# Optimization experiments

Hardware: AMD Instinct MI355X
Metric: run time of the kernel (lower is better)

The kernel has to match this reference:

```python
import jax, jax.numpy as jnp
import numpy as np

B, N, DIM, H, DH, MLP, L = 4, 1024, 1024, 16, 64, 4096, 2
C = DIM // 4  # conditioning dim = 256


def setup_inputs() -> dict:
    key = jax.random.key(0)
    ks = jax.random.split(key, 12)
    s = 0.02
    return dict(
        x=jax.random.normal(ks[0], (B, N, DIM), jnp.float32),
        mu=jax.random.normal(ks[1], (B, N, C), jnp.float32),
        f=jax.random.normal(ks[2], (B, N, C), jnp.float32),
        Wqkv=jax.random.normal(ks[3], (L, DIM, 3 * H * DH), jnp.float32) * s,
        Wout=jax.random.normal(ks[4], (L, H * DH, DIM), jnp.float32) * s,
        bout=jnp.zeros((L, DIM), jnp.float32),
        W1=jax.random.normal(ks[5], (L, DIM, MLP), jnp.float32) * s,
        b1=jnp.zeros((L, MLP), jnp.float32),
        W2=jax.random.normal(ks[6], (L, MLP, DIM), jnp.float32) * s,
        b2=jnp.zeros((L, DIM), jnp.float32),
        Wmu=jax.random.normal(ks[7], (L, C, 6 * C), jnp.float32) * s,
        bmu=jnp.zeros((L, 6 * C), jnp.float32),
        Wf=jax.random.normal(ks[8], (L, C, 6 * 3 * C), jnp.float32) * s,
        bf=jnp.zeros((L, 6 * 3 * C), jnp.float32),
        g1=jnp.ones((L, DIM), jnp.float32),
        be1=jnp.zeros((L, DIM), jnp.float32),
        g2=jnp.ones((L, DIM), jnp.float32),
        be2=jnp.zeros((L, DIM), jnp.float32),
    )


def _ln(x, g, b):
    m = jnp.mean(x, -1, keepdims=True)
    v = jnp.mean((x - m) ** 2, -1, keepdims=True)
    return (x - m) * jax.lax.rsqrt(v + 1e-5) * g + b


def reference(x, mu, f, Wqkv, Wout, bout, W1, b1, W2, b2, Wmu, bmu, Wf, bf, g1, be1, g2, be2):
    scale = DH ** -0.5
    smu = jax.nn.silu(mu)  # SiLU applied to raw conditioning, shared across layers
    sf = jax.nn.silu(f)
    for i in range(L):
        mm = smu @ Wmu[i] + bmu[i]          # [B,N,6*C]
        mf = sf @ Wf[i] + bf[i]             # [B,N,6*3*C]
        mus = jnp.split(mm, 6, axis=-1)     # each [B,N,C]
        fs = jnp.split(mf, 6, axis=-1)      # each [B,N,3C]
        sh_a, sc_a, ga_a, sh_m, sc_m, ga_m = [
            jnp.concatenate([a, b_], -1) for a, b_ in zip(mus, fs)
        ]                                   # each [B,N,DIM]
        # attention branch
        h = _ln(x, g1[i], be1[i]) * (1 + sc_a) + sh_a
        qkv = h @ Wqkv[i]                   # [B,N,3*H*DH]
        q, k, v = [t.reshape(B, N, H, DH) for t in jnp.split(qkv, 3, axis=-1)]
        att = jax.nn.softmax(jnp.einsum('bihd,bjhd->bhij', q, k) * scale, axis=-1)
        o = jnp.einsum('bhij,bjhd->bihd', att, v).reshape(B, N, H * DH)
        x = x + ga_a * (o @ Wout[i] + bout[i])
        # MLP branch
        h2 = _ln(x, g2[i], be2[i]) * (1 + sc_m) + sh_m
        mlp = jax.nn.gelu(h2 @ W1[i] + b1[i], approximate=False) @ W2[i] + b2[i]
        x = x + ga_m * mlp
    return x
```

## Files before the change

kernel.cpp:

```cpp
#include <hip/hip_runtime.h>
#include <math.h>

#define BB 4
#define NN 1024
#define DIMD 1024
#define HHN 16
#define DHH 64
#define MLPD 4096
#define LLN 2
#define CCD 256
#define BNROWS (BB*NN)

typedef __attribute__((ext_vector_type(8))) _Float16 h8;
typedef __attribute__((ext_vector_type(4))) _Float16 h4;
typedef __attribute__((ext_vector_type(4))) float f32x4;

#define GLD16(gp, lp) __builtin_amdgcn_global_load_lds( \
    (const __attribute__((address_space(1))) void*)(gp), \
    (__attribute__((address_space(3))) void*)(lp), 16, 0, 0)

__global__ __launch_bounds__(256) void silu_kernel(const float* __restrict__ in,
                                                   _Float16* __restrict__ out, int n4) {
  int i = blockIdx.x * 256 + threadIdx.x;
  if (i < n4) {
    float4 v = ((const float4*)in)[i];
    h4 o;
    o[0] = (_Float16)(v.x / (1.f + __expf(-v.x)));
    o[1] = (_Float16)(v.y / (1.f + __expf(-v.y)));
    o[2] = (_Float16)(v.z / (1.f + __expf(-v.z)));
    o[3] = (_Float16)(v.w / (1.f + __expf(-v.w)));
    ((h4*)out)[i] = o;
  }
}

__global__ __launch_bounds__(256) void transpose_cast(const float* __restrict__ in,
                                                      _Float16* __restrict__ out,
                                                      int K, int N) {
  __shared__ float tile[32][33];
  int bx = blockIdx.x * 32;
  int by = blockIdx.y * 32;
  int tx = threadIdx.x, ty = threadIdx.y;
  #pragma unroll
  for (int r = 0; r < 32; r += 8)
    tile[ty + r][tx] = in[(size_t)(by + ty + r) * N + bx + tx];
  __syncthreads();
  #pragma unroll
  for (int r = 0; r < 32; r += 8)
    out[(size_t)(bx + ty + r) * K + by + tx] = (_Float16)tile[tx][ty + r];
}

template <int EPI, int BNT>
__global__ __launch_bounds__(256) void gemm_bt(
    const _Float16* __restrict__ A, const _Float16* __restrict__ Bt,
    int M, int Nt, int K,
    const float* __restrict__ bias,
    _Float16* __restrict__ outh,
    float* __restrict__ xio,
    const _Float16* __restrict__ mmb, const _Float16* __restrict__ mfb, int gchunk) {
  constexpr int NREP = BNT / 32;
  __shared__ _Float16 As[2][128 * 32];
  __shared__ _Float16 Bs[2][BNT * 32];
  const int tid = threadIdx.x;
  const int wave = tid >> 6, lane = tid & 63;
  const int brow = blockIdx.x * 128, bcol = blockIdx.y * BNT;
  const int wr = (wave >> 1) * 64, wc = (wave & 1) * (BNT / 2);
  const int r = lane & 15, g = lane >> 4;
  f32x4 acc[4][NREP];
  #pragma unroll
  for (int m = 0; m < 4; m++)
    #pragma unroll
    for (int n = 0; n < NREP; n++) acc[m][n] = (f32x4){0.f, 0.f, 0.f, 0.f};

  const _Float16* gA = A + (size_t)(brow + wave * 32 + (lane >> 2)) * K + (lane & 3) * 8;
  const _Float16* gB = Bt + (size_t)(bcol + wave * (BNT / 4) + (lane >> 2)) * K + (lane & 3) * 8;

  auto STAGE = [&](int b, int k0) {
    GLD16(gA + k0, &As[b][wave * 1024]);
    GLD16(gA + k0 + 16 * (size_t)K, &As[b][wave * 1024 + 512]);
    if (BNT == 128) {
      GLD16(gB + k0, &Bs[b][wave * 1024]);
      GLD16(gB + k0 + 16 * (size_t)K, &Bs[b][wave * 1024 + 512]);
    } else {
      GLD16(gB + k0, &Bs[b][wave * 512]);
    }
  };

  STAGE(0, 0);
  int cur = 0;
  for (int k0 = 0; k0 < K; k0 += 32) {
    __syncthreads();
    if (k0 + 32 < K) STAGE(cur ^ 1, k0 + 32);
    h8 af[4], bfr[NREP];
    #pragma unroll
    for (int m = 0; m < 4; m++) af[m] = *(const h8*)(&As[cur][(wr + m * 16 + r) * 32 + g * 8]);
    #pragma unroll
    for (int n = 0; n < NREP; n++) bfr[n] = *(const h8*)(&Bs[cur][(wc + n * 16 + r) * 32 + g * 8]);
    #pragma unroll
    for (int m = 0; m < 4; m++)
      #pragma unroll
      for (int n = 0; n < NREP; n++)
        acc[m][n] = __builtin_amdgcn_mfma_f32_16x16x32_f16(af[m], bfr[n], acc[m][n], 0, 0, 0);
    cur ^= 1;
  }

  #pragma unroll
  for (int n = 0; n < NREP; n++) {
    const int gcol = bcol + wc + n * 16 + r;
    const float bv = bias ? bias[gcol] : 0.f;
    #pragma unroll
    for (int m = 0; m < 4; m++) {
      const int growb = brow + wr + m * 16 + 4 * g;
      #pragma unroll
      for (int q = 0; q < 4; q++) {
        float v = acc[m][n][q] + bv;
        const size_t grow = (size_t)(growb + q);
        if (EPI == 0) {
          outh[grow * Nt + gcol] = (_Float16)v;
        } else if (EPI == 1) {
          float t = 0.5f * v * (1.f + erff(v * 0.70710678118f));
          outh[grow * Nt + gcol] = (_Float16)t;
        } else {
          float gaw = (gcol < CCD)
              ? (float)mmb[grow * (6 * CCD) + gchunk * CCD + gcol]
              : (float)mfb[grow * (18 * CCD) + gchunk * (3 * CCD) + (gcol - CCD)];
          xio[grow * DIMD + gcol] += gaw * v;
        }
      }
    }
  }
}

__global__ __launch_bounds__(256) void ln_mod(const float* __restrict__ x,
                                              const float* __restrict__ gam,
                                              const float* __restrict__ bet,
                                              const _Float16* __restrict__ mmb,
                                              const _Float16* __restrict__ mfb,
                                              int jsh, int jsc,
                                              _Float16* __restrict__ hout) {
  const int row = blockIdx.x;
  const int tid = threadIdx.x;
  const float* xr = x + (size_t)row * DIMD;
  float4 v = ((const float4*)xr)[tid];
  float s = v.x + v.y + v.z + v.w;
  float sq = v.x * v.x + v.y * v.y + v.z * v.z + v.w * v.w;
  #pragma unroll
  for (int off = 32; off > 0; off >>= 1) {
    s += __shfl_down(s, off);
    sq += __shfl_down(sq, off);
  }
  __shared__ float red[8];
  int wv = tid >> 6, ln = tid & 63;
  if (ln == 0) { red[wv] = s; red[4 + wv] = sq; }
  __syncthreads();
  s = red[0] + red[1] + red[2] + red[3];
  sq = red[4] + red[5] + red[6] + red[7];
  float mean = s * (1.f / DIMD);
  float var = sq * (1.f / DIMD) - mean * mean;
  float rs = rsqrtf(var + 1e-5f);
  int c0 = tid * 4;
  float4 gm = ((const float4*)gam)[tid];
  float4 bt = ((const float4*)bet)[tid];
  float xv[4] = {v.x, v.y, v.z, v.w};
  float gv[4] = {gm.x, gm.y, gm.z, gm.w};
  float bv[4] = {bt.x, bt.y, bt.z, bt.w};
  h4 o;
  #pragma unroll
  for (int i = 0; i < 4; i++) {
    int c = c0 + i;
    float lnv = (xv[i] - mean) * rs * gv[i] + bv[i];
    float shv, scv;
    if (c < CCD) {
      shv = (float)mmb[(size_t)row * (6 * CCD) + jsh * CCD + c];
      scv = (float)mmb[(size_t)row * (6 * CCD) + jsc * CCD + c];
    } else {
      shv = (float)mfb[(size_t)row * (18 * CCD) + jsh * (3 * CCD) + (c - CCD)];
      scv = (float)mfb[(size_t)row * (18 * CCD) + jsc * (3 * CCD) + (c - CCD)];
    }
    o[i] = (_Float16)(lnv * (1.f + scv) + shv);
  }
  *((h4*)(hout + (size_t)row * DIMD + c0)) = o;
}

__global__ __launch_bounds__(256) void attn_kernel(const _Float16* __restrict__ qkv,
                                                   _Float16* __restrict__ o) {
  __shared__ _Float16 Vs[64 * 64];
  __shared__ _Float16 Ps[4][16 * 72];
  const int bh = blockIdx.y;
  const int b = bh >> 4, hh = bh & 15;
  const int tid = threadIdx.x;
  const int wave = tid >> 6, lane = tid & 63;
  const int r = lane & 15, g = lane >> 4;
  const int RS = 3 * HHN * DHH;
  const _Float16* qb = qkv + (size_t)b * NN * RS + hh * DHH;
  const _Float16* kb = qb + HHN * DHH;
  const _Float16* vb = qb + 2 * HHN * DHH;
  const int q0 = blockIdx.x * 64 + wave * 16;

  h8 qf[2];
  qf[0] = *(const h8*)(qb + (size_t)(q0 + r) * RS + g * 8);
  qf[1] = *(const h8*)(qb + (size_t)(q0 + r) * RS + 32 + g * 8);

  f32x4 oacc[4];
  #pragma unroll
  for (int n = 0; n < 4; n++) oacc[n] = (f32x4){0.f, 0.f, 0.f, 0.f};
  float mrun[4] = {-1e30f, -1e30f, -1e30f, -1e30f};
  float lrun[4] = {0.f, 0.f, 0.f, 0.f};
  const float scale = 0.125f;

  for (int kt = 0; kt < NN / 64; ++kt) {
    const int k0 = kt * 64;
    __syncthreads();
    {
      int id = wave * 64 + lane;
      GLD16(vb + (size_t)(k0 + (id >> 3)) * RS + (id & 7) * 8, Vs + wave * 512);
      int id2 = id + 256;
      GLD16(vb + (size_t)(k0 + (id2 >> 3)) * RS + (id2 & 7) * 8, Vs + 2048 + wave * 512);
    }
    f32x4 sfr[4];
    #pragma unroll
    for (int n = 0; n < 4; n++) sfr[n] = (f32x4){0.f, 0.f, 0.f, 0.f};
    #pragma unroll
    for (int n = 0; n < 4; n++) {
      h8 kf0 = *(const h8*)(kb + (size_t)(k0 + n * 16 + r) * RS + g * 8);
      h8 kf1 = *(const h8*)(kb + (size_t)(k0 + n * 16 + r) * RS + 32 + g * 8);
      sfr[n] = __builtin_amdgcn_mfma_f32_16x16x32_f16(qf[0], kf0, sfr[n], 0, 0, 0);
      sfr[n] = __builtin_amdgcn_mfma_f32_16x16x32_f16(qf[1], kf1, sfr[n], 0, 0, 0);
    }
    float pm[4];
    #pragma unroll
    for (int q = 0; q < 4; q++)
      pm[q] = fmaxf(fmaxf(sfr[0][q], sfr[1][q]), fmaxf(sfr[2][q], sfr[3][q])) * scale;
    #pragma unroll
    for (int off = 1; off < 16; off <<= 1)
      #pragma unroll
      for (int q = 0; q < 4; q++) pm[q] = fmaxf(pm[q], __shfl_xor(pm[q], off));
    float fac[4], rsum[4];
    #pragma unroll
    for (int q = 0; q < 4; q++) {
      float mn = fmaxf(mrun[q], pm[q]);
      fac[q] = __expf(mrun[q] - mn);
      mrun[q] = mn;
      rsum[q] = 0.f;
    }
    #pragma unroll
    for (int n = 0; n < 4; n++)
      #pragma unroll
      for (int q = 0; q < 4; q++) {
        float p = __expf(sfr[n][q] * scale - mrun[q]);
        sfr[n][q] = p;
        rsum[q] += p;
      }
    #pragma unroll
    for (int off = 1; off < 16; off <<= 1)
      #pragma unroll
      for (int q = 0; q < 4; q++) rsum[q] += __shfl_xor(rsum[q], off);
    #pragma unroll
    for (int q = 0; q < 4; q++) lrun[q] = lrun[q] * fac[q] + rsum[q];
    #pragma unroll
    for (int n = 0; n < 4; n++)
      #pragma unroll
      for (int q = 0; q < 4; q++) oacc[n][q] *= fac[q];
    _Float16* Pw = Ps[wave];
    #pragma unroll
    for (int n = 0; n < 4; n++)
      #pragma unroll
      for (int q = 0; q < 4; q++)
        Pw[(4 * g + q) * 72 + n * 16 + r] = (_Float16)sfr[n][q];
    __syncthreads();
    h8 pa[2];
    pa[0] = *(const h8*)(Pw + r * 72 + g * 8);
    pa[1] = *(const h8*)(Pw + r * 72 + 32 + g * 8);
    #pragma unroll
    for (int nd = 0; nd < 4; nd++) {
      #pragma unroll
      for (int c = 0; c < 2; c++) {
        h8 vf;
        #pragma unroll
        for (int j = 0; j < 8; j++) vf[j] = Vs[(c * 32 + 8 * g + j) * 64 + nd * 16 + r];
        oacc[nd] = __builtin_amdgcn_mfma_f32_16x16x32_f16(pa[c], vf, oacc[nd], 0, 0, 0);
      }
    }
  }
  #pragma unroll
  for (int nd = 0; nd < 4; nd++)
    #pragma unroll
    for (int q = 0; q < 4; q++) {
      int row = q0 + 4 * g + q;
      int col = hh * DHH + nd * 16 + r;
      o[((size_t)b * NN + row) * DIMD + col] = (_Float16)(oacc[nd][q] / lrun[q]);
    }
}

extern "C" void kernel_launch(void* const* d_in, const int* in_sizes, int n_in,
                              void* d_out, int out_size, void* d_ws, size_t ws_size,
                              hipStream_t stream) {
  (void)in_sizes; (void)n_in; (void)out_size; (void)ws_size;
  const float* mu   = (const float*)d_in[1];
  const float* f_in = (const float*)d_in[2];
  const float* Wqkv = (const float*)d_in[3];
  const float* Wout = (const float*)d_in[4];
  const float* bout = (const float*)d_in[5];
  const float* W1   = (const float*)d_in[6];
  const float* b1   = (const float*)d_in[7];
  const float* W2   = (const float*)d_in[8];
  const float* b2   = (const float*)d_in[9];
  const float* Wmu  = (const float*)d_in[10];
  const float* bmu  = (const float*)d_in[11];
  const float* Wf   = (const float*)d_in[12];
  const float* bfv  = (const float*)d_in[13];
  const float* g1   = (const float*)d_in[14];
  const float* be1  = (const float*)d_in[15];
  const float* g2   = (const float*)d_in[16];
  const float* be2  = (const float*)d_in[17];
  float* xout = (float*)d_out;

  char* ws = (char*)d_ws;
  size_t off = 0;
  auto alloc = [&](size_t elems) -> _Float16* {
    _Float16* p = (_Float16*)(ws + off);
    off += ((elems * 2 + 255) / 256) * 256;
    return p;
  };
  _Float16* wTqkv = alloc((size_t)LLN * 3072 * 1024);
  _Float16* wTout = alloc((size_t)LLN * 1024 * 1024);
  _Float16* wT1   = alloc((size_t)LLN * 4096 * 1024);
  _Float16* wT2   = alloc((size_t)LLN * 1024 * 4096);
  _Float16* wTmu  = alloc((size_t)LLN * 1536 * 256);
  _Float16* wTf   = alloc((size_t)LLN * 4608 * 256);
  _Float16* smu   = alloc((size_t)BNROWS * CCD);
  _Float16* sfb   = alloc((size_t)BNROWS * CCD);
  _Float16* mmb   = alloc((size_t)BNROWS * 6 * CCD);
  _Float16* mfb   = alloc((size_t)BNROWS * 18 * CCD);
  _Float16* hbuf  = alloc((size_t)BNROWS * DIMD);
  _Float16* qkvb  = alloc((size_t)BNROWS * 3 * DIMD);
  _Float16* obuf  = alloc((size_t)BNROWS * DIMD);
  _Float16* m1b   = alloc((size_t)BNROWS * MLPD);

  hipMemcpyAsync(d_out, d_in[0], (size_t)BNROWS * DIMD * sizeof(float),
                 hipMemcpyDeviceToDevice, stream);

  silu_kernel<<<BNROWS * CCD / 4 / 256, 256, 0, stream>>>(mu, smu, BNROWS * CCD / 4);
  silu_kernel<<<BNROWS * CCD / 4 / 256, 256, 0, stream>>>(f_in, sfb, BNROWS * CCD / 4);

  dim3 tb(32, 8);
  for (int l = 0; l < LLN; l++) {
    transpose_cast<<<dim3(3072 / 32, 1024 / 32), tb, 0, stream>>>(
        Wqkv + (size_t)l * 1024 * 3072, wTqkv + (size_t)l * 3072 * 1024, 1024, 3072);
    transpose_cast<<<dim3(1024 / 32, 1024 / 32), tb, 0, stream>>>(
        Wout + (size_t)l * 1024 * 1024, wTout + (size_t)l * 1024 * 1024, 1024, 1024);
    transpose_cast<<<dim3(4096 / 32, 1024 / 32), tb, 0, stream>>>(
        W1 + (size_t)l * 1024 * 4096, wT1 + (size_t)l * 4096 * 1024, 1024, 4096);
    transpose_cast<<<dim3(1024 / 32, 4096 / 32), tb, 0, stream>>>(
        W2 + (size_t)l * 4096 * 1024, wT2 + (size_t)l * 1024 * 4096, 4096, 1024);
    transpose_cast<<<dim3(1536 / 32, 256 / 32), tb, 0, stream>>>(
        Wmu + (size_t)l * 256 * 1536, wTmu + (size_t)l * 1536 * 256, 256, 1536);
    transpose_cast<<<dim3(4608 / 32, 256 / 32), tb, 0, stream>>>(
        Wf + (size_t)l * 256 * 4608, wTf + (size_t)l * 4608 * 256, 256, 4608);
  }

  for (int l = 0; l < LLN; l++) {
    gemm_bt<0, 64><<<dim3(BNROWS / 128, 1536 / 64), 256, 0, stream>>>(
        smu, wTmu + (size_t)l * 1536 * 256, BNROWS, 1536, 256,
        bmu + (size_t)l * 1536, mmb, nullptr, nullptr, nullptr, 0);
    gemm_bt<0, 128><<<dim3(BNROWS / 128, 4608 / 128), 256, 0, stream>>>(
        sfb, wTf + (size_t)l * 4608 * 256, BNROWS, 4608, 256,
        bfv + (size_t)l * 4608, mfb, nullptr, nullptr, nullptr, 0);
    ln_mod<<<BNROWS, 256, 0, stream>>>(xout, g1 + (size_t)l * DIMD, be1 + (size_t)l * DIMD,
                                       mmb, mfb, 0, 1, hbuf);
    gemm_bt<0, 128><<<dim3(BNROWS / 128, 3072 / 128), 256, 0, stream>>>(
        hbuf, wTqkv + (size_t)l * 3072 * 1024, BNROWS, 3072, 1024,
        nullptr, qkvb, nullptr, nullptr, nullptr, 0);
    attn_kernel<<<dim3(NN / 64, BB * HHN), 256, 0, stream>>>(qkvb, obuf);
    gemm_bt<2, 64><<<dim3(BNROWS / 128, 1024 / 64), 256, 0, stream>>>(
        obuf, wTout + (size_t)l * 1024 * 1024, BNROWS, 1024, 1024,
        bout + (size_t)l * DIMD, nullptr, xout, mmb, mfb, 2);
    ln_mod<<<BNROWS, 256, 0, stream>>>(xout, g2 + (size_t)l * DIMD, be2 + (size_t)l * DIMD,
                                       mmb, mfb, 3, 4, hbuf);
    gemm_bt<1, 128><<<dim3(BNROWS / 128, 4096 / 128), 256, 0, stream>>>(
        hbuf, wT1 + (size_t)l * 4096 * 1024, BNROWS, 4096, 1024,
        b1 + (size_t)l * MLPD, m1b, nullptr, nullptr, nullptr, 0);
    gemm_bt<2, 64><<<dim3(BNROWS / 128, 1024 / 64), 256, 0, stream>>>(
        m1b, wT2 + (size_t)l * 1024 * 4096, BNROWS, 1024, 4096,
        b2 + (size_t)l * DIMD, nullptr, xout, mmb, mfb, 5);
  }
}
```

Measured before the change: 760.0 us.

## Pre-transpose V for attention and vectorize weight transpose-cast kernel

Adds a v_transpose kernel that writes V per head in a [d][n] layout. The attention kernel can then load V MFMA fragments straight from global memory as contiguous h8 vectors. This removes the per-tile LDS staging of V, the scalar gathers from LDS, and both block-wide __syncthreads per key tile. The weight transpose_cast kernel also moves to 64x64 tiles with float4 loads and h4 stores. The cost is an extra kernel launch and an extra write and read of V per layer, and V fragments now come from global memory or cache instead of LDS.

Result: slower. 819.2 us (+7.8%).

```diff
diff --git a/kernel.cpp b/kernel.cpp
--- a/kernel.cpp
+++ b/kernel.cpp
@@ -36,17 +36,46 @@
 __global__ __launch_bounds__(256) void transpose_cast(const float* __restrict__ in,
                                                       _Float16* __restrict__ out,
                                                       int K, int N) {
-  __shared__ float tile[32][33];
-  int bx = blockIdx.x * 32;
-  int by = blockIdx.y * 32;
-  int tx = threadIdx.x, ty = threadIdx.y;
-  #pragma unroll
-  for (int r = 0; r < 32; r += 8)
-    tile[ty + r][tx] = in[(size_t)(by + ty + r) * N + bx + tx];
+  __shared__ float tile[64][68];
+  int bx = blockIdx.x * 64;
+  int by = blockIdx.y * 64;
+  int tid = threadIdx.x;
+  int r0 = tid >> 4, c4 = (tid & 15) * 4;
+  #pragma unroll
+  for (int i = 0; i < 4; i++) {
+    float4 v = *(const float4*)(in + (size_t)(by + r0 + i * 16) * N + bx + c4);
+    *(float4*)&tile[r0 + i * 16][c4] = v;
+  }
   __syncthreads();
   #pragma unroll
-  for (int r = 0; r < 32; r += 8)
-    out[(size_t)(bx + ty + r) * K + by + tx] = (_Float16)tile[tx][ty + r];
+  for (int i = 0; i < 4; i++) {
+    int orow = r0 + i * 16;
+    h4 o;
+    #pragma unroll
+    for (int j = 0; j < 4; j++) o[j] = (_Float16)tile[c4 + j][orow];
+    *(h4*)(out + (size_t)(bx + orow) * K + by + c4) = o;
+  }
+}
+
+__global__ __launch_bounds__(256) void v_transpose(const _Float16* __restrict__ qkv,
+                                                   _Float16* __restrict__ vt) {
+  __shared__ _Float16 t[64][72];
+  int n0 = blockIdx.x * 64;
+  int bh = blockIdx.y;
+  int b = bh >> 4;
+  const _Float16* src = qkv + (size_t)b * NN * 3072 + 2048 + (bh & 15) * 64;
+  int tid = threadIdx.x;
+  int row = tid >> 2, c0 = (tid & 3) * 16;
+  *(h8*)&t[row][c0] = *(const h8*)(src + (size_t)(n0 + row) * 3072 + c0);
+  *(h8*)&t[row][c0 + 8] = *(const h8*)(src + (size_t)(n0 + row) * 3072 + c0 + 8);
+  __syncthreads();
+  int d = tid >> 2, ns = (tid & 3) * 16;
+  h8 o0, o1;
+  #pragma unroll
+  for (int j = 0; j < 8; j++) { o0[j] = t[ns + j][d]; o1[j] = t[ns + 8 + j][d]; }
+  _Float16* dst = vt + ((size_t)bh * 64 + d) * NN + n0 + ns;
+  *(h8*)dst = o0;
+  *(h8*)(dst + 8) = o1;
 }
 
 template <int EPI, int BNT>
@@ -182,8 +211,8 @@
 }
 
 __global__ __launch_bounds__(256) void attn_kernel(const _Float16* __restrict__ qkv,
+                                                   const _Float16* __restrict__ vt,
                                                    _Float16* __restrict__ o) {
-  __shared__ _Float16 Vs[64 * 64];
   __shared__ _Float16 Ps[4][16 * 72];
   const int bh = blockIdx.y;
   const int b = bh >> 4, hh = bh & 15;
@@ -193,7 +222,7 @@
   const int RS = 3 * HHN * DHH;
   const _Float16* qb = qkv + (size_t)b * NN * RS + hh * DHH;
   const _Float16* kb = qb + HHN * DHH;
-  const _Float16* vb = qb + 2 * HHN * DHH;
+  const _Float16* vtb = vt + (size_t)bh * DHH * NN;
   const int q0 = blockIdx.x * 64 + wave * 16;
 
   h8 qf[2];
@@ -206,16 +235,10 @@
   float mrun[4] = {-1e30f, -1e30f, -1e30f, -1e30f};
   float lrun[4] = {0.f, 0.f, 0.f, 0.f};
   const float scale = 0.125f;
+  _Float16* Pw = Ps[wave];
 
   for (int kt = 0; kt < NN / 64; ++kt) {
     const int k0 = kt * 64;
-    __syncthreads();
-    {
-      int id = wave * 64 + lane;
-      GLD16(vb + (size_t)(k0 + (id >> 3)) * RS + (id & 7) * 8, Vs + wave * 512);
-      int id2 = id + 256;
-      GLD16(vb + (size_t)(k0 + (id2 >> 3)) * RS + (id2 & 7) * 8, Vs + 2048 + wave * 512);
-    }
     f32x4 sfr[4];
     #pragma unroll
     for (int n = 0; n < 4; n++) sfr[n] = (f32x4){0.f, 0.f, 0.f, 0.f};
@@ -260,13 +283,11 @@
     for (int n = 0; n < 4; n++)
       #pragma unroll
       for (int q = 0; q < 4; q++) oacc[n][q] *= fac[q];
-    _Float16* Pw = Ps[wave];
     #pragma unroll
     for (int n = 0; n < 4; n++)
       #pragma unroll
       for (int q = 0; q < 4; q++)
         Pw[(4 * g + q) * 72 + n * 16 + r] = (_Float16)sfr[n][q];
-    __syncthreads();
     h8 pa[2];
     pa[0] = *(const h8*)(Pw + r * 72 + g * 8);
     pa[1] = *(const h8*)(Pw + r * 72 + 32 + g * 8);
@@ -274,9 +295,7 @@
     for (int nd = 0; nd < 4; nd++) {
       #pragma unroll
       for (int c = 0; c < 2; c++) {
-        h8 vf;
-        #pragma unroll
-        for (int j = 0; j < 8; j++) vf[j] = Vs[(c * 32 + 8 * g + j) * 64 + nd * 16 + r];
+        h8 vf = *(const h8*)(vtb + (size_t)(nd * 16 + r) * NN + k0 + c * 32 + g * 8);
         oacc[nd] = __builtin_amdgcn_mfma_f32_16x16x32_f16(pa[c], vf, oacc[nd], 0, 0, 0);
       }
     }
@@ -335,6 +354,7 @@
   _Float16* qkvb  = alloc((size_t)BNROWS * 3 * DIMD);
   _Float16* obuf  = alloc((size_t)BNROWS * DIMD);
   _Float16* m1b   = alloc((size_t)BNROWS * MLPD);
+  _Float16* vtb   = alloc((size_t)BNROWS * DIMD);
 
   hipMemcpyAsync(d_out, d_in[0], (size_t)BNROWS * DIMD * sizeof(float),
                  hipMemcpyDeviceToDevice, stream);
@@ -342,19 +362,18 @@
   silu_kernel<<<BNROWS * CCD / 4 / 256, 256, 0, stream>>>(mu, smu, BNROWS * CCD / 4);
   silu_kernel<<<BNROWS * CCD / 4 / 256, 256, 0, stream>>>(f_in, sfb, BNROWS * CCD / 4);
 
-  dim3 tb(32, 8);
   for (int l = 0; l < LLN; l++) {
-    transpose_cast<<<dim3(3072 / 32, 1024 / 32), tb, 0, stream>>>(
+    transpose_cast<<<dim3(3072 / 64, 1024 / 64), 256, 0, stream>>>(
         Wqkv + (size_t)l * 1024 * 3072, wTqkv + (size_t)l * 3072 * 1024, 1024, 3072);
-    transpose_cast<<<dim3(1024 / 32, 1024 / 32), tb, 0, stream>>>(
+    transpose_cast<<<dim3(1024 / 64, 1024 / 64), 256, 0, stream>>>(
         Wout + (size_t)l * 1024 * 1024, wTout + (size_t)l * 1024 * 1024, 1024, 1024);
-    transpose_cast<<<dim3(4096 / 32, 1024 / 32), tb, 0, stream>>>(
+    transpose_cast<<<dim3(4096 / 64, 1024 / 64), 256, 0, stream>>>(
         W1 + (size_t)l * 1024 * 4096, wT1 + (size_t)l * 4096 * 1024, 1024, 4096);
-    transpose_cast<<<dim3(1024 / 32, 4096 / 32), tb, 0, stream>>>(
+    transpose_cast<<<dim3(1024 / 64, 4096 / 64), 256, 0, stream>>>(
         W2 + (size_t)l * 4096 * 1024, wT2 + (size_t)l * 1024 * 4096, 4096, 1024);
-    transpose_cast<<<dim3(1536 / 32, 256 / 32), tb, 0, stream>>>(
+    transpose_cast<<<dim3(1536 / 64, 256 / 64), 256, 0, stream>>>(
         Wmu + (size_t)l * 256 * 1536, wTmu + (size_t)l * 1536 * 256, 256, 1536);
-    transpose_cast<<<dim3(4608 / 32, 256 / 32), tb, 0, stream>>>(
+    transpose_cast<<<dim3(4608 / 64, 256 / 64), 256, 0, stream>>>(
         Wf + (size_t)l * 256 * 4608, wTf + (size_t)l * 4608 * 256, 256, 4608);
   }
 
@@ -370,7 +389,8 @@
     gemm_bt<0, 128><<<dim3(BNROWS / 128, 3072 / 128), 256, 0, stream>>>(
         hbuf, wTqkv + (size_t)l * 3072 * 1024, BNROWS, 3072, 1024,
         nullptr, qkvb, nullptr, nullptr, nullptr, 0);
-    attn_kernel<<<dim3(NN / 64, BB * HHN), 256, 0, stream>>>(qkvb, obuf);
+    v_transpose<<<dim3(NN / 64, BB * HHN), 256, 0, stream>>>(qkvb, vtb);
+    attn_kernel<<<dim3(NN / 64, BB * HHN), 256, 0, stream>>>(qkvb, vtb, obuf);
     gemm_bt<2, 64><<<dim3(BNROWS / 128, 1024 / 64), 256, 0, stream>>>(
         obuf, wTout + (size_t)l * 1024 * 1024, BNROWS, 1024, 1024,
         bout + (size_t)l * DIMD, nullptr, xout, mmb, mfb, 2);
```
